# Optimization experiments

Measured on AMD Instinct MI355X. Metric: run time of the kernel, lower is better.

The kernel has to match this reference:

```python
import jax, jax.numpy as jnp
import numpy as np
import math

NUM_HEADS = 4
HIDDEN = 256
HEAD_DIM = HIDDEN // NUM_HEADS
NEG = jnp.finfo(jnp.float32).min


def setup_inputs() -> dict:
    key = jax.random.key(0)
    ks = jax.random.split(key, 8)
    B, Q, K = 4, 2048, 2048
    q_hidden_states = jax.random.normal(ks[0], (B, Q, HIDDEN), dtype=jnp.float32)
    k_hidden_states = jax.random.normal(ks[1], (B, K, HIDDEN), dtype=jnp.float32)
    attention_mask = jnp.zeros((B, 1, Q, K), dtype=jnp.float32)
    align_mask = jax.random.randint(ks[2], (B, K, Q), 0, 2, dtype=jnp.int32)
    s = 1.0 / math.sqrt(HIDDEN)
    Wq = jax.random.normal(ks[3], (HIDDEN, HIDDEN), dtype=jnp.float32) * s
    Wk = jax.random.normal(ks[4], (HIDDEN, HIDDEN), dtype=jnp.float32) * s
    Wv = jax.random.normal(ks[5], (HIDDEN, HIDDEN), dtype=jnp.float32) * s
    Wo = jax.random.normal(ks[6], (HIDDEN, HIDDEN), dtype=jnp.float32) * s
    return {"q_hidden_states": q_hidden_states, "k_hidden_states": k_hidden_states,
            "attention_mask": attention_mask, "align_mask": align_mask,
            "Wq": Wq, "Wk": Wk, "Wv": Wv, "Wo": Wo}


def reference(q_hidden_states, k_hidden_states, attention_mask, align_mask, Wq, Wk, Wv, Wo):
    B, Q, _ = q_hidden_states.shape
    K = k_hidden_states.shape[1]
    # torch Linear: y = x @ W.T  -> [B, S, H, D]
    q = (q_hidden_states @ Wq.T).reshape(B, Q, NUM_HEADS, HEAD_DIM)
    k = (k_hidden_states @ Wk.T).reshape(B, K, NUM_HEADS, HEAD_DIM)
    v = (k_hidden_states @ Wv.T).reshape(B, K, NUM_HEADS, HEAD_DIM)
    # scores: [B, H, Q, K]
    scores = jnp.einsum('bqhd,bkhd->bhqk', q, k) / math.sqrt(HEAD_DIM)
    # additive mask + clamp to finfo min
    scores = jnp.maximum(scores + attention_mask, NEG)
    # align_mask: (B, K, Q) -> (B, 1, Q, K); masked_fill where == 0
    am = jnp.transpose(align_mask, (0, 2, 1))[:, None, :, :]
    scores = jnp.where(am == 0, NEG, scores)
    scores = jnp.maximum(scores, NEG)
    probs = jax.nn.softmax(scores.astype(jnp.float32), axis=-1).astype(q.dtype)
    attn = jnp.einsum('bhqk,bkhd->bqhd', probs, v).reshape(B, Q, HIDDEN)
    return attn @ Wo.T
```

## Files before the change

kernel.cpp:

```cpp
#include <hip/hip_runtime.h>

#define NEGF -3.402823466e38f
#define MASKED_F -3.38953139e38f
#define LOG2E 1.44269504088896f

typedef __attribute__((ext_vector_type(8))) short bf16x8;
typedef __attribute__((ext_vector_type(4))) float f32x4;
typedef __attribute__((ext_vector_type(4))) unsigned short u16x4;

__device__ __forceinline__ unsigned short f2bf(float f) {
  unsigned u = __builtin_bit_cast(unsigned, f);
  u += 0x7fffu + ((u >> 16) & 1u);
  return (unsigned short)(u >> 16);
}

#define GLOAD_LDS16(gsrc, ldst)                                                     \
  __builtin_amdgcn_global_load_lds(                                                 \
      (const __attribute__((address_space(1))) void*)(gsrc),                        \
      (__attribute__((address_space(3))) void*)(ldst), 16, 0, 0)

#define OFF_QH  0u
#define OFF_KH  2097152u
#define OFF_W   4194304u
#define OFF_QP  4456448u
#define OFF_KP  6553600u
#define OFF_VT  8650752u
#define OFF_ATT 10747904u
#define OFF_M   12845056u
#define USHORT_USED 29622272u

__global__ __launch_bounds__(256) void k_convert(
    const float* __restrict__ qh, const float* __restrict__ kh,
    const float* __restrict__ w0, const float* __restrict__ w1,
    const float* __restrict__ w2, const float* __restrict__ w3,
    unsigned short* __restrict__ dst) {
  int v = blockIdx.x * 256 + threadIdx.x;
  const float* src;
  if (v < 524288)       src = qh + (size_t)v * 4;
  else if (v < 1048576) src = kh + ((size_t)v - 524288) * 4;
  else {
    int t = v - 1048576;
    int which = t >> 14;
    const float* w = (which == 0) ? w0 : (which == 1) ? w1 : (which == 2) ? w2 : w3;
    src = w + (size_t)(t & 16383) * 4;
  }
  f32x4 x = *(const f32x4*)src;
  u16x4 o;
  o[0] = f2bf(x[0]); o[1] = f2bf(x[1]); o[2] = f2bf(x[2]); o[3] = f2bf(x[3]);
  *(u16x4*)(dst + (size_t)v * 4) = o;
}

__global__ __launch_bounds__(256) void k_maskprep(const float* __restrict__ am,
    const int* __restrict__ al, unsigned short* __restrict__ M) {
  __shared__ float L[64 * 65];
  int bid = blockIdx.x;
  int b = bid >> 10, q64 = (bid >> 5) & 31, k64 = bid & 31;
  int t = threadIdx.x, c = t & 63, rg = t >> 6;

  const float* amb = am + ((size_t)b * 2048 + q64 * 64) * 2048 + k64 * 64;
#pragma unroll
  for (int i = 0; i < 16; ++i) {
    int row = i * 4 + rg;
    L[row * 65 + c] = amb[(size_t)row * 2048 + c] * LOG2E;
  }
  __syncthreads();
  const int* alb = al + ((size_t)b * 2048 + k64 * 64) * 2048 + q64 * 64;
#pragma unroll
  for (int i = 0; i < 16; ++i) {
    int kr = i * 4 + rg;
    if (alb[(size_t)kr * 2048 + c] == 0) L[c * 65 + kr] = MASKED_F;
  }
  __syncthreads();
  int w = t >> 6, lane = t & 63, l15 = lane & 15, l4 = lane >> 4;
  unsigned short* outp = M + ((((size_t)(b * 128 + q64 * 4 + w)) * 32 + k64) * 64 + lane) * 16;
#pragma unroll
  for (int kt = 0; kt < 4; ++kt) {
    u16x4 o;
#pragma unroll
    for (int r = 0; r < 4; ++r)
      o[r] = f2bf(L[(w * 16 + l4 * 4 + r) * 65 + kt * 16 + l15]);
    *(u16x4*)(outp + kt * 4) = o;
  }
}

__global__ __launch_bounds__(256) void k_proj(unsigned short* __restrict__ ws) {
  int bid = blockIdx.x;
  int mat = bid / 512;
  int rem = bid - mat * 512;
  int mt = rem >> 2, nt = rem & 3;
  int tid = threadIdx.x, w = tid >> 6, lane = tid & 63;
  int l15 = lane & 15, l4 = lane >> 4;

  const unsigned short* X = ws + (mat == 0 ? OFF_QH : OFF_KH);
  const unsigned short* W = ws + OFF_W + (size_t)mat * 65536;

  int i0 = mt * 64 + w * 16;
  int arow = i0 + l15;
  int koff = l4 * 8;

  f32x4 acc[4] = {};
  for (int ks = 0; ks < 8; ++ks) {
    bf16x8 a = *(const bf16x8*)(X + (size_t)arow * 256 + ks * 32 + koff);
#pragma unroll
    for (int ct = 0; ct < 4; ++ct) {
      bf16x8 bb = *(const bf16x8*)(W + (size_t)(nt * 64 + ct * 16 + l15) * 256 + ks * 32 + koff);
      acc[ct] = __builtin_amdgcn_mfma_f32_16x16x32_bf16(a, bb, acc[ct], 0, 0, 0);
    }
  }

  unsigned short* Qp = ws + OFF_QP;
  unsigned short* Kp = ws + OFF_KP;
  unsigned short* Vt = ws + OFF_VT;
  int rbase = i0 + l4 * 4;
#pragma unroll
  for (int ct = 0; ct < 4; ++ct) {
#pragma unroll
    for (int r = 0; r < 4; ++r) {
      int row = rbase + r;
      int b = row >> 11, s = row & 2047;
      int d = ct * 16 + l15;
      float v = acc[ct][r];
      if (mat == 0)      Qp[((size_t)(b * 4 + nt) * 2048 + s) * 64 + d] = f2bf(v * (0.125f * LOG2E));
      else if (mat == 1) Kp[((size_t)(b * 4 + nt) * 2048 + s) * 64 + d] = f2bf(v);
      else               Vt[((size_t)(b * 4 + nt) * 64 + d) * 2048 + s] = f2bf(v);
    }
  }
}

template <int NS>
__global__ __launch_bounds__(256) void k_attn(unsigned short* __restrict__ ws,
    float* __restrict__ po, float* __restrict__ pm, float* __restrict__ pl) {
  constexpr int LOG = (NS == 4) ? 2 : (NS == 2) ? 1 : 0;
  constexpr int SPAN = 2048 / NS;

  __shared__ __align__(16) unsigned short Kb[2][4096];
  __shared__ __align__(16) unsigned short Vb[2][4096];
  __shared__ __align__(16) unsigned short plds[4][1024];

  int bid = blockIdx.x;
  int sp = bid & (NS - 1);
  int qt = (bid >> LOG) & 31;
  int bh = bid >> (LOG + 5);
  int b = bh >> 2, h = bh & 3;
  int tid = threadIdx.x, w = tid >> 6, lane = tid & 63;
  int l15 = lane & 15, l4 = lane >> 4;
  int q0 = qt * 64 + w * 16;

  const unsigned short* Qp = ws + OFF_QP;
  const unsigned short* Kp = ws + OFF_KP + (size_t)bh * 2048 * 64;
  const unsigned short* Vt = ws + OFF_VT + (size_t)bh * 64 * 2048;
  const unsigned short* Mw = ws + OFF_M +
      (((size_t)(b * 128 + qt * 4 + w)) * 32) * 1024 + (size_t)lane * 16;

  int srow = lane >> 3;
  int scol = ((lane & 7) ^ srow) * 8;
  int c0 = w * 2;

  bf16x8 qf0 = *(const bf16x8*)(Qp + ((size_t)bh * 2048 + q0 + l15) * 64 + l4 * 8);
  bf16x8 qf1 = *(const bf16x8*)(Qp + ((size_t)bh * 2048 + q0 + l15) * 64 + 32 + l4 * 8);

  f32x4 o[4] = {};
  float mrun[4] = {-__builtin_inff(), -__builtin_inff(), -__builtin_inff(), -__builtin_inff()};
  float lrun[4] = {0.f, 0.f, 0.f, 0.f};

  int kk0 = sp * SPAN;
#pragma unroll
  for (int c2 = 0; c2 < 2; ++c2) {
    int c = c0 + c2;
    GLOAD_LDS16(Kp + (size_t)(kk0 + c * 8 + srow) * 64 + scol, &Kb[0][c * 512]);
    GLOAD_LDS16(Vt + (size_t)(c * 8 + srow) * 2048 + kk0 + scol, &Vb[0][c * 512]);
  }
  __syncthreads();

  int cur = 0;
  for (int kk = kk0; kk < kk0 + SPAN; kk += 64) {
    if (kk + 64 < kk0 + SPAN) {
#pragma unroll
      for (int c2 = 0; c2 < 2; ++c2) {
        int c = c0 + c2;
        GLOAD_LDS16(Kp + (size_t)(kk + 64 + c * 8 + srow) * 64 + scol, &Kb[cur ^ 1][c * 512]);
        GLOAD_LDS16(Vt + (size_t)(c * 8 + srow) * 2048 + (kk + 64) + scol, &Vb[cur ^ 1][c * 512]);
      }
    }
    const unsigned short* mp = Mw + ((size_t)(kk >> 6)) * 1024;
    bf16x8 m0 = *(const bf16x8*)mp;
    bf16x8 m1 = *(const bf16x8*)(mp + 8);

    f32x4 sfr[4];
    __builtin_amdgcn_s_setprio(1);
#pragma unroll
    for (int kt = 0; kt < 4; ++kt) {
      int row = kt * 16 + l15;
      int sw = l15 & 7;
      bf16x8 k0 = *(const bf16x8*)&Kb[cur][row * 64 + ((l4 ^ sw) * 8)];
      bf16x8 k1 = *(const bf16x8*)&Kb[cur][row * 64 + (((4 + l4) ^ sw) * 8)];
      f32x4 acc = {};
      acc = __builtin_amdgcn_mfma_f32_16x16x32_bf16(qf0, k0, acc, 0, 0, 0);
      acc = __builtin_amdgcn_mfma_f32_16x16x32_bf16(qf1, k1, acc, 0, 0, 0);
      sfr[kt] = acc;
    }
    __builtin_amdgcn_s_setprio(0);

#pragma unroll
    for (int kt = 0; kt < 4; ++kt) {
#pragma unroll
      for (int r = 0; r < 4; ++r) {
        int j = kt * 4 + r;
        unsigned short mu = (unsigned short)(j < 8 ? m0[j] : m1[j & 7]);
        float madd = __builtin_bit_cast(float, (unsigned)mu << 16);
        sfr[kt][r] = fmaxf(sfr[kt][r] + madd, NEGF);
      }
    }
    float mnew[4], sfac[4];
#pragma unroll
    for (int r = 0; r < 4; ++r) {
      float rm = fmaxf(fmaxf(sfr[0][r], sfr[1][r]), fmaxf(sfr[2][r], sfr[3][r]));
      rm = fmaxf(rm, __shfl_xor(rm, 1));
      rm = fmaxf(rm, __shfl_xor(rm, 2));
      rm = fmaxf(rm, __shfl_xor(rm, 4));
      rm = fmaxf(rm, __shfl_xor(rm, 8));
      mnew[r] = fmaxf(mrun[r], rm);
      sfac[r] = exp2f(mrun[r] - mnew[r]);
      mrun[r] = mnew[r];
    }
#pragma unroll
    for (int kt = 0; kt < 4; ++kt)
#pragma unroll
      for (int r = 0; r < 4; ++r)
        sfr[kt][r] = exp2f(sfr[kt][r] - mnew[r]);
#pragma unroll
    for (int r = 0; r < 4; ++r) {
      float rs = sfr[0][r] + sfr[1][r] + sfr[2][r] + sfr[3][r];
      rs += __shfl_xor(rs, 1);
      rs += __shfl_xor(rs, 2);
      rs += __shfl_xor(rs, 4);
      rs += __shfl_xor(rs, 8);
      lrun[r] = lrun[r] * sfac[r] + rs;
      o[0][r] *= sfac[r]; o[1][r] *= sfac[r]; o[2][r] *= sfac[r]; o[3][r] *= sfac[r];
    }
#pragma unroll
    for (int kt = 0; kt < 4; ++kt)
#pragma unroll
      for (int r = 0; r < 4; ++r) {
        int prow = l4 * 4 + r;
        int pcol = kt * 16 + l15;
        plds[w][prow * 64 + (((pcol >> 3) ^ (prow & 7)) << 3) + (pcol & 7)] = f2bf(sfr[kt][r]);
      }
    __builtin_amdgcn_s_setprio(1);
#pragma unroll
    for (int ks = 0; ks < 2; ++ks) {
      int chnk = ks * 4 + l4;
      bf16x8 pa = *(const bf16x8*)&plds[w][l15 * 64 + ((chnk ^ (l15 & 7)) << 3)];
#pragma unroll
      for (int dt = 0; dt < 4; ++dt) {
        int row = dt * 16 + l15;
        bf16x8 vf = *(const bf16x8*)&Vb[cur][row * 64 + (((ks * 4 + l4) ^ (l15 & 7)) * 8)];
        o[dt] = __builtin_amdgcn_mfma_f32_16x16x32_bf16(pa, vf, o[dt], 0, 0, 0);
      }
    }
    __builtin_amdgcn_s_setprio(0);

    __syncthreads();
    cur ^= 1;
  }

  if constexpr (NS == 1) {
    unsigned short* attnb = ws + OFF_ATT;
#pragma unroll
    for (int r = 0; r < 4; ++r) {
      float inv = 1.0f / lrun[r];
      int qrow = q0 + l4 * 4 + r;
#pragma unroll
      for (int dt = 0; dt < 4; ++dt)
        attnb[(size_t)(b * 2048 + qrow) * 256 + h * 64 + dt * 16 + l15] = f2bf(o[dt][r] * inv);
    }
  } else {
    float* pob = po + (((size_t)sp * 16 + bh) * 2048) * 64;
#pragma unroll
    for (int r = 0; r < 4; ++r) {
      int qrow = q0 + l4 * 4 + r;
#pragma unroll
      for (int dt = 0; dt < 4; ++dt)
        pob[(size_t)qrow * 64 + dt * 16 + l15] = o[dt][r];
      if (l15 == 0) {
        pm[(size_t)sp * 32768 + bh * 2048 + qrow] = mrun[r];
        pl[(size_t)sp * 32768 + bh * 2048 + qrow] = lrun[r];
      }
    }
  }
}

template <int NS>
__global__ __launch_bounds__(256) void k_combine(const float* __restrict__ po,
    const float* __restrict__ pm, const float* __restrict__ pl,
    unsigned short* __restrict__ attnb) {
  int t = blockIdx.x * 256 + threadIdx.x;
  int d = t & 63;
  int row = t >> 6;

  float m[NS], l[NS];
  float M = -__builtin_inff();
#pragma unroll
  for (int sp = 0; sp < NS; ++sp) {
    m[sp] = pm[(size_t)sp * 32768 + row];
    l[sp] = pl[(size_t)sp * 32768 + row];
    M = fmaxf(M, m[sp]);
  }
  float denom = 0.f, acc = 0.f;
#pragma unroll
  for (int sp = 0; sp < NS; ++sp) {
    float wgt = exp2f(m[sp] - M);
    denom += l[sp] * wgt;
    acc += po[((size_t)sp * 32768 + row) * 64 + d] * wgt;
  }
  float val = acc / denom;
  int bh = row >> 11, qrow = row & 2047;
  int b = bh >> 2, h = bh & 3;
  attnb[((size_t)(b * 2048 + qrow)) * 256 + h * 64 + d] = f2bf(val);
}

__global__ __launch_bounds__(256) void k_oproj(const unsigned short* __restrict__ ws,
                                               float* __restrict__ out) {
  int bid = blockIdx.x;
  int mt = bid >> 2, nt = bid & 3;
  int tid = threadIdx.x, w = tid >> 6, lane = tid & 63;
  int l15 = lane & 15, l4 = lane >> 4;

  const unsigned short* A = ws + OFF_ATT;
  const unsigned short* W = ws + OFF_W + 3u * 65536u;
  int i0 = mt * 64 + w * 16;

  f32x4 acc[4] = {};
  for (int ks = 0; ks < 8; ++ks) {
    bf16x8 a = *(const bf16x8*)(A + (size_t)(i0 + l15) * 256 + ks * 32 + l4 * 8);
#pragma unroll
    for (int ct = 0; ct < 4; ++ct) {
      bf16x8 bb = *(const bf16x8*)(W + (size_t)(nt * 64 + ct * 16 + l15) * 256 + ks * 32 + l4 * 8);
      acc[ct] = __builtin_amdgcn_mfma_f32_16x16x32_bf16(a, bb, acc[ct], 0, 0, 0);
    }
  }
#pragma unroll
  for (int ct = 0; ct < 4; ++ct)
#pragma unroll
    for (int r = 0; r < 4; ++r)
      out[(size_t)(i0 + l4 * 4 + r) * 256 + nt * 64 + ct * 16 + l15] = acc[ct][r];
}

extern "C" void kernel_launch(void* const* d_in, const int* in_sizes, int n_in,
                              void* d_out, int out_size, void* d_ws, size_t ws_size,
                              hipStream_t stream) {
  const float* qh = (const float*)d_in[0];
  const float* kh = (const float*)d_in[1];
  const float* amask = (const float*)d_in[2];
  const int* alignm = (const int*)d_in[3];
  const float* Wq = (const float*)d_in[4];
  const float* Wk = (const float*)d_in[5];
  const float* Wv = (const float*)d_in[6];
  const float* Wo = (const float*)d_in[7];
  float* out = (float*)d_out;
  unsigned short* ws = (unsigned short*)d_ws;

  k_convert<<<4352, 256, 0, stream>>>(qh, kh, Wq, Wk, Wv, Wo, ws);
  k_maskprep<<<4096, 256, 0, stream>>>(amask, alignm, ws + OFF_M);
  k_proj<<<1536, 256, 0, stream>>>(ws);

  size_t avail_f = (ws_size > (size_t)USHORT_USED * 2)
                       ? (ws_size - (size_t)USHORT_USED * 2) / 4 : 0;
  auto need = [](int ns) { return (size_t)ns * (2097152 + 65536); };
  int NSv = (avail_f >= need(2)) ? 2 : 1;
  float* po = (float*)(ws + USHORT_USED);
  float* pm = po + (size_t)NSv * 2097152;
  float* pl = pm + (size_t)NSv * 32768;

  if (NSv == 2) {
    k_attn<2><<<1024, 256, 0, stream>>>(ws, po, pm, pl);
    k_combine<2><<<8192, 256, 0, stream>>>(po, pm, pl, ws + OFF_ATT);
  } else {
    k_attn<1><<<512, 256, 0, stream>>>(ws, po, pm, pl);
  }
  k_oproj<<<512, 256, 0, stream>>>(ws, out);
}
```

Baseline: 152.8 us.

## Transpose score MFMA layout and defer softmax rescaling in flash attention

Swaps the MFMA operands so each lane holds one query row's scores, which reduces row-max and row-sum to two cross-lane shuffles and lets the sum accumulate per lane until the end. Adds lazy rescaling: the running max and output accumulators are only updated when some row's new max exceeds the old one by a threshold, which skips exp and multiply work on most tiles. Also packs the P tile into LDS with a hardware bf16 pack instruction and 8-byte stores, and changes the mask prepack layout to match the transposed fragment. The cost is the extra shuffles needed to broadcast rescale factors and the risk of precision loss when exponents are allowed to grow up to 2^8.

Result: faster. 132.3 us (-13.4%).

```diff
diff --git a/kernel.cpp b/kernel.cpp
--- a/kernel.cpp
+++ b/kernel.cpp
@@ -3,10 +3,12 @@
 #define NEGF -3.402823466e38f
 #define MASKED_F -3.38953139e38f
 #define LOG2E 1.44269504088896f
+#define DEFER_THR 8.0f
 
 typedef __attribute__((ext_vector_type(8))) short bf16x8;
 typedef __attribute__((ext_vector_type(4))) float f32x4;
 typedef __attribute__((ext_vector_type(4))) unsigned short u16x4;
+typedef __attribute__((ext_vector_type(2))) unsigned int u32x2;
 
 __device__ __forceinline__ unsigned short f2bf(float f) {
   unsigned u = __builtin_bit_cast(unsigned, f);
@@ -78,7 +80,7 @@
     u16x4 o;
 #pragma unroll
     for (int r = 0; r < 4; ++r)
-      o[r] = f2bf(L[(w * 16 + l4 * 4 + r) * 65 + kt * 16 + l15]);
+      o[r] = f2bf(L[(w * 16 + l15) * 65 + kt * 16 + l4 * 4 + r]);
     *(u16x4*)(outp + kt * 4) = o;
   }
 }
@@ -160,8 +162,8 @@
   bf16x8 qf1 = *(const bf16x8*)(Qp + ((size_t)bh * 2048 + q0 + l15) * 64 + 32 + l4 * 8);
 
   f32x4 o[4] = {};
-  float mrun[4] = {-__builtin_inff(), -__builtin_inff(), -__builtin_inff(), -__builtin_inff()};
-  float lrun[4] = {0.f, 0.f, 0.f, 0.f};
+  float mrun = -__builtin_inff();
+  float lpart = 0.f;
 
   int kk0 = sp * SPAN;
 #pragma unroll
@@ -195,57 +197,63 @@
       bf16x8 k0 = *(const bf16x8*)&Kb[cur][row * 64 + ((l4 ^ sw) * 8)];
       bf16x8 k1 = *(const bf16x8*)&Kb[cur][row * 64 + (((4 + l4) ^ sw) * 8)];
       f32x4 acc = {};
-      acc = __builtin_amdgcn_mfma_f32_16x16x32_bf16(qf0, k0, acc, 0, 0, 0);
-      acc = __builtin_amdgcn_mfma_f32_16x16x32_bf16(qf1, k1, acc, 0, 0, 0);
+      acc = __builtin_amdgcn_mfma_f32_16x16x32_bf16(k0, qf0, acc, 0, 0, 0);
+      acc = __builtin_amdgcn_mfma_f32_16x16x32_bf16(k1, qf1, acc, 0, 0, 0);
       sfr[kt] = acc;
     }
     __builtin_amdgcn_s_setprio(0);
 
 #pragma unroll
-    for (int kt = 0; kt < 4; ++kt) {
+    for (int kt = 0; kt < 4; ++kt)
 #pragma unroll
       for (int r = 0; r < 4; ++r) {
         int j = kt * 4 + r;
         unsigned short mu = (unsigned short)(j < 8 ? m0[j] : m1[j & 7]);
-        float madd = __builtin_bit_cast(float, (unsigned)mu << 16);
-        sfr[kt][r] = fmaxf(sfr[kt][r] + madd, NEGF);
-      }
-    }
-    float mnew[4], sfac[4];
-#pragma unroll
-    for (int r = 0; r < 4; ++r) {
-      float rm = fmaxf(fmaxf(sfr[0][r], sfr[1][r]), fmaxf(sfr[2][r], sfr[3][r]));
-      rm = fmaxf(rm, __shfl_xor(rm, 1));
-      rm = fmaxf(rm, __shfl_xor(rm, 2));
-      rm = fmaxf(rm, __shfl_xor(rm, 4));
-      rm = fmaxf(rm, __shfl_xor(rm, 8));
-      mnew[r] = fmaxf(mrun[r], rm);
-      sfac[r] = exp2f(mrun[r] - mnew[r]);
-      mrun[r] = mnew[r];
-    }
+        sfr[kt][r] += __builtin_bit_cast(float, (unsigned)mu << 16);
+      }
+
+    float pmax = sfr[0][0];
 #pragma unroll
     for (int kt = 0; kt < 4; ++kt)
 #pragma unroll
-      for (int r = 0; r < 4; ++r)
-        sfr[kt][r] = exp2f(sfr[kt][r] - mnew[r]);
-#pragma unroll
-    for (int r = 0; r < 4; ++r) {
-      float rs = sfr[0][r] + sfr[1][r] + sfr[2][r] + sfr[3][r];
-      rs += __shfl_xor(rs, 1);
-      rs += __shfl_xor(rs, 2);
-      rs += __shfl_xor(rs, 4);
-      rs += __shfl_xor(rs, 8);
-      lrun[r] = lrun[r] * sfac[r] + rs;
-      o[0][r] *= sfac[r]; o[1][r] *= sfac[r]; o[2][r] *= sfac[r]; o[3][r] *= sfac[r];
-    }
+      for (int r = 0; r < 4; ++r) pmax = fmaxf(pmax, sfr[kt][r]);
+    pmax = fmaxf(pmax, __shfl_xor(pmax, 16));
+    pmax = fmaxf(pmax, __shfl_xor(pmax, 32));
+
+    if (__any(pmax > mrun + DEFER_THR)) {
+      float mnew = fmaxf(mrun, pmax);
+      float sfac = exp2f(mrun - mnew);
+      mrun = mnew;
+      lpart *= sfac;
+#pragma unroll
+      for (int r = 0; r < 4; ++r) {
+        float sf = __shfl(sfac, l4 * 4 + r);
+        o[0][r] *= sf; o[1][r] *= sf; o[2][r] *= sf; o[3][r] *= sf;
+      }
+    }
+
+    float ls = 0.f;
 #pragma unroll
     for (int kt = 0; kt < 4; ++kt)
 #pragma unroll
       for (int r = 0; r < 4; ++r) {
-        int prow = l4 * 4 + r;
-        int pcol = kt * 16 + l15;
-        plds[w][prow * 64 + (((pcol >> 3) ^ (prow & 7)) << 3) + (pcol & 7)] = f2bf(sfr[kt][r]);
-      }
+        float e = exp2f(sfr[kt][r] - mrun);
+        sfr[kt][r] = e;
+        ls += e;
+      }
+    lpart += ls;
+
+#pragma unroll
+    for (int kt = 0; kt < 4; ++kt) {
+      unsigned lo, hi;
+      asm("v_cvt_pk_bf16_f32 %0, %1, %2" : "=v"(lo) : "v"(sfr[kt][0]), "v"(sfr[kt][1]));
+      asm("v_cvt_pk_bf16_f32 %0, %1, %2" : "=v"(hi) : "v"(sfr[kt][2]), "v"(sfr[kt][3]));
+      int chunk = kt * 2 + (l4 >> 1);
+      int addr = l15 * 64 + (((chunk) ^ (l15 & 7)) << 3) + ((l4 & 1) << 2);
+      u32x2 pk; pk[0] = lo; pk[1] = hi;
+      *(u32x2*)&plds[w][addr] = pk;
+    }
+
     __builtin_amdgcn_s_setprio(1);
 #pragma unroll
     for (int ks = 0; ks < 2; ++ks) {
@@ -264,11 +272,15 @@
     cur ^= 1;
   }
 
+  float lsum = lpart;
+  lsum += __shfl_xor(lsum, 16);
+  lsum += __shfl_xor(lsum, 32);
+
   if constexpr (NS == 1) {
     unsigned short* attnb = ws + OFF_ATT;
 #pragma unroll
     for (int r = 0; r < 4; ++r) {
-      float inv = 1.0f / lrun[r];
+      float inv = 1.0f / __shfl(lsum, l4 * 4 + r);
       int qrow = q0 + l4 * 4 + r;
 #pragma unroll
       for (int dt = 0; dt < 4; ++dt)
@@ -282,10 +294,10 @@
 #pragma unroll
       for (int dt = 0; dt < 4; ++dt)
         pob[(size_t)qrow * 64 + dt * 16 + l15] = o[dt][r];
-      if (l15 == 0) {
-        pm[(size_t)sp * 32768 + bh * 2048 + qrow] = mrun[r];
-        pl[(size_t)sp * 32768 + bh * 2048 + qrow] = lrun[r];
-      }
+    }
+    if (l4 == 0) {
+      pm[(size_t)sp * 32768 + bh * 2048 + q0 + l15] = mrun;
+      pl[(size_t)sp * 32768 + bh * 2048 + q0 + l15] = lsum;
     }
   }
 }
```
